# Kernel optimization log

Hardware: AMD Instinct MI355X
Metric: run time of the kernel (lower is better)

## Reference

```python
import jax, jax.numpy as jnp
import numpy as np


def _l2norm(t, axis=-1, eps=1e-12):
    # matches torch F.normalize: x / max(||x||, eps)
    n = jnp.sqrt(jnp.sum(t * t, axis=axis, keepdims=True))
    return t / jnp.maximum(n, eps)


def setup_inputs() -> dict:
    key = jax.random.key(0)
    ks = jax.random.split(key, 5)
    B, N, C, H = 16, 4096, 768, 12
    x = jax.random.normal(ks[0], (B, N, C), dtype=jnp.float32)
    Wqkv = jax.random.normal(ks[1], (C, 3 * C), dtype=jnp.float32) * (C ** -0.5)
    bqkv = jax.random.normal(ks[2], (3 * C,), dtype=jnp.float32) * 0.02
    Wproj = jax.random.normal(ks[3], (C, C), dtype=jnp.float32) * (C ** -0.5)
    bproj = jax.random.normal(ks[4], (C,), dtype=jnp.float32) * 0.02
    temperature = jnp.ones((H, 1, 1), dtype=jnp.float32)
    return {"x": x, "Wqkv": Wqkv, "bqkv": bqkv, "Wproj": Wproj,
            "bproj": bproj, "temperature": temperature}


def reference(x, Wqkv, bqkv, Wproj, bproj, temperature):
    B, N, C = x.shape
    H = temperature.shape[0]
    Dh = C // H
    qkv = x @ Wqkv + bqkv                      # [B,N,3C]
    qkv = qkv.reshape(B, N, 3, H, Dh)
    # -> [3,B,H,Dh,N] (channels-as-tokens layout)
    qkv = jnp.transpose(qkv, (2, 0, 3, 4, 1))
    q, k, v = qkv[0], qkv[1], qkv[2]           # each [B,H,Dh,N]
    q = _l2norm(q, axis=-1)
    k = _l2norm(k, axis=-1)
    # cross-covariance over channels: [B,H,Dh,Dh]
    attn = jnp.einsum('bhdn,bhen->bhde', q, k) * temperature
    attn = jax.nn.softmax(attn, axis=-1)
    out = jnp.einsum('bhde,bhen->bhdn', attn, v)  # [B,H,Dh,N]
    out = jnp.transpose(out, (0, 3, 1, 2)).reshape(B, N, C)
    return out @ Wproj + bproj
```

## Files before the change

kernel.cpp:

```cpp
#include <hip/hip_runtime.h>

typedef __bf16 bf16x8 __attribute__((ext_vector_type(8)));
typedef float  f32x4  __attribute__((ext_vector_type(4)));
typedef unsigned short u16x8 __attribute__((ext_vector_type(8)));
typedef unsigned short u16x4 __attribute__((ext_vector_type(4)));

#define MFMA16(a, b, c) __builtin_amdgcn_mfma_f32_16x16x32_bf16((a), (b), (c), 0, 0, 0)

#define GLOAD16(g, l) __builtin_amdgcn_global_load_lds( \
    (const __attribute__((address_space(1))) void*)(g),  \
    (__attribute__((address_space(3))) void*)(l), 16, 0, 0)

__device__ __forceinline__ float bf2f(unsigned short u) {
    unsigned int x = ((unsigned int)u) << 16;
    return __builtin_bit_cast(float, x);
}
__device__ __forceinline__ unsigned short f2bf(float f) {
    unsigned int x = __builtin_bit_cast(unsigned int, f);
    x = x + 0x7FFFu + ((x >> 16) & 1u);
    return (unsigned short)(x >> 16);
}
__device__ __forceinline__ bool is_f32(const unsigned short* tf) { return tf[0] == 0; }
__device__ __forceinline__ float ldscal(const void* p, int i, bool f32m) {
    return f32m ? ((const float*)p)[i] : bf2f(((const unsigned short*)p)[i]);
}

__global__ __launch_bounds__(256)
void tr_dual(const void* __restrict__ in_, unsigned short* __restrict__ xb,
             unsigned short* __restrict__ xbT, float* __restrict__ sB,
             const unsigned short* __restrict__ tf)
{
    __shared__ unsigned short T[64 * 72];
    const bool f32m = is_f32(tf);
    const int tx = blockIdx.x % 12;
    const int ty = blockIdx.x / 12;
    const int r0 = ty * 64, c0 = tx * 64;
    const int t = threadIdx.x;
#pragma unroll
    for (int s = 0; s < 2; ++s) {
        const int idx = t + s * 256;
        const int rr = idx >> 3;
        const int cc = (idx & 7) * 8;
        u16x8 v;
        if (f32m) {
            const float* inf = (const float*)in_;
            f32x4 a = *(const f32x4*)&inf[(size_t)(r0 + rr) * 768 + c0 + cc];
            f32x4 b = *(const f32x4*)&inf[(size_t)(r0 + rr) * 768 + c0 + cc + 4];
#pragma unroll
            for (int j = 0; j < 4; ++j) { v[j] = f2bf(a[j]); v[4 + j] = f2bf(b[j]); }
        } else {
            v = *(const u16x8*)&((const unsigned short*)in_)[(size_t)(r0 + rr) * 768 + c0 + cc];
        }
        *(u16x8*)&xb[(size_t)(r0 + rr) * 768 + c0 + cc] = v;
#pragma unroll
        for (int j = 0; j < 8; ++j) T[(cc + j) * 72 + rr] = v[j];
    }
    __syncthreads();
#pragma unroll
    for (int s = 0; s < 2; ++s) {
        const int idx = t + s * 256;
        const int cc = idx >> 3;
        const int rr = (idx & 7) * 8;
        u16x8 v = *(const u16x8*)&T[cc * 72 + rr];
        *(u16x8*)&xbT[(size_t)(c0 + cc) * 65536 + r0 + rr] = v;
    }
    {
        const int col = t >> 2;
        const int seg = t & 3;
        float s = 0.f;
#pragma unroll
        for (int r = 0; r < 16; ++r) s += bf2f(T[col * 72 + seg * 16 + r]);
        s += __shfl_xor(s, 1);
        s += __shfl_xor(s, 2);
        if (seg == 0) atomicAdd(&sB[(r0 >> 12) * 768 + c0 + col], s);
    }
}

__device__ __forceinline__ void tr_tile(const void* in_, unsigned short* out,
                                        int R, int C, int istride,
                                        int bid, bool f32m, unsigned short* T)
{
    const int nct = C >> 6;
    const int tx = bid % nct;
    const int ty = bid / nct;
    const int r0 = ty * 64, c0 = tx * 64;
    const int t = threadIdx.x;
#pragma unroll
    for (int s = 0; s < 2; ++s) {
        const int idx = t + s * 256;
        const int rr = idx >> 3;
        const int cc = (idx & 7) * 8;
        unsigned short v[8];
        if (f32m) {
            const float* inf = (const float*)in_;
            f32x4 a = *(const f32x4*)&inf[(size_t)(r0 + rr) * istride + c0 + cc];
            f32x4 b = *(const f32x4*)&inf[(size_t)(r0 + rr) * istride + c0 + cc + 4];
#pragma unroll
            for (int j = 0; j < 4; ++j) { v[j] = f2bf(a[j]); v[4 + j] = f2bf(b[j]); }
        } else {
            u16x8 a = *(const u16x8*)&((const unsigned short*)in_)[(size_t)(r0 + rr) * istride + c0 + cc];
#pragma unroll
            for (int j = 0; j < 8; ++j) v[j] = a[j];
        }
#pragma unroll
        for (int j = 0; j < 8; ++j) T[(cc + j) * 72 + rr] = v[j];
    }
    __syncthreads();
#pragma unroll
    for (int s = 0; s < 2; ++s) {
        const int idx = t + s * 256;
        const int cc = idx >> 3;
        const int rr = (idx & 7) * 8;
        u16x8 v = *(const u16x8*)&T[cc * 72 + rr];
        *(u16x8*)&out[(size_t)(c0 + cc) * R + r0 + rr] = v;
    }
}

__global__ __launch_bounds__(256)
void wprep(const void* __restrict__ Wqkv, const void* __restrict__ Wp,
           unsigned short* __restrict__ WqkT, unsigned short* __restrict__ Wv_bf,
           unsigned short* __restrict__ WprojT, const unsigned short* __restrict__ tf)
{
    __shared__ unsigned short T[64 * 72];
    const bool f32m = is_f32(tf);
    const int bid = blockIdx.x;
    if (bid < 288) {
        tr_tile(Wqkv, WqkT, 768, 1536, 2304, bid, f32m, T);
    } else if (bid < 576) {
        const int t = (bid - 288) * 256 + threadIdx.x;
        const int c = t / 96;
        const int e0 = (t % 96) * 8;
        u16x8 v;
        if (f32m) {
            const float* p = (const float*)Wqkv + (size_t)c * 2304 + 1536 + e0;
            f32x4 a = *(const f32x4*)p;
            f32x4 b = *(const f32x4*)(p + 4);
#pragma unroll
            for (int j = 0; j < 4; ++j) { v[j] = f2bf(a[j]); v[4 + j] = f2bf(b[j]); }
        } else {
            v = *(const u16x8*)&((const unsigned short*)Wqkv)[(size_t)c * 2304 + 1536 + e0];
        }
        *(u16x8*)&Wv_bf[(size_t)c * 768 + e0] = v;
    } else {
        tr_tile(Wp, WprojT, 768, 768, 768, bid - 576, f32m, T);
    }
}

template<int MODE>
__global__ __launch_bounds__(512, 2)
void gemm2ph(const unsigned short* __restrict__ A,
             const unsigned short* __restrict__ BT,
             const float* __restrict__ bias,
             unsigned short* __restrict__ o0,
             float* __restrict__ oF,
             const unsigned short* __restrict__ tf)
{
    constexpr int K = 768, NT = 12;
    __shared__ __align__(16) char SM[131072];
    unsigned short* lds = (unsigned short*)SM;

    const bool f32m = is_f32(tf);
    const int tid  = threadIdx.x;
    const int wave = tid >> 6;
    const int lane = tid & 63;
    const int wm   = wave >> 2;
    const int wn   = wave & 3;
    const int lr   = lane & 15;
    const int lq   = lane >> 4;

    const int per = gridDim.x >> 3;
    const int wg  = (blockIdx.x & 7) * per + (blockIdx.x >> 3);
    int b = 0, mt, nt;
    if (MODE == 4) { b = wg / 18; const int r = wg % 18; mt = r / 3; nt = r % 3; }
    else           { mt = wg / 3; nt = wg % 3; }
    const size_t m0 = (size_t)mt * 256;
    const int n0 = nt * 256;

    const unsigned short* Ab = A + m0 * K;
    const unsigned short* Bb;
    if (MODE == 1)      Bb = BT + (m0 >> 12) * (size_t)589824 + (size_t)n0 * K;
    else if (MODE == 4) Bb = BT + (size_t)b * 589824 + (size_t)n0 * K;
    else                Bb = BT + (size_t)n0 * K;

    f32x4 zero = {0.f, 0.f, 0.f, 0.f};
    f32x4 acc[8][4];
#pragma unroll
    for (int i = 0; i < 8; ++i)
#pragma unroll
        for (int j = 0; j < 4; ++j) acc[i][j] = zero;

    auto STAGE = [&](int t) {
        unsigned short* la_ = lds + (t & 1) * 32768;
        unsigned short* lb_ = la_ + 16384;
        const unsigned short* ga = Ab + t * 64;
        const unsigned short* gb = Bb + t * 64;
#pragma unroll
        for (int it = 0; it < 4; ++it) {
            const int c = it * 512 + tid;
            const int row = c >> 3;
            const int gs = (c & 7) ^ (row & 7);
            GLOAD16(ga + (size_t)row * K + gs * 8, la_ + c * 8);
        }
#pragma unroll
        for (int it = 0; it < 4; ++it) {
            const int c = it * 512 + tid;
            const int row = c >> 3;
            const int gs = (c & 7) ^ (row & 7);
            GLOAD16(gb + (size_t)row * K + gs * 8, lb_ + c * 8);
        }
    };

    STAGE(0);
    STAGE(1);

    for (int t = 0; t < NT; ++t) {
        if (t + 1 < NT) asm volatile("s_waitcnt vmcnt(8)" ::: "memory");
        else            asm volatile("s_waitcnt vmcnt(0)" ::: "memory");
        __builtin_amdgcn_s_barrier();
        __builtin_amdgcn_sched_barrier(0);

        const char* la = (const char*)(lds + (t & 1) * 32768);
        const char* lb = la + 32768;

        bf16x8 bfr[4][2];
#pragma unroll
        for (int ni = 0; ni < 4; ++ni)
#pragma unroll
            for (int ks = 0; ks < 2; ++ks) {
                const int row = wn * 64 + ni * 16 + lr;
                const int s   = ks * 4 + lq;
                bfr[ni][ks] = *(const bf16x8*)(lb + row * 128 + ((s ^ (row & 7)) << 4));
            }
#pragma unroll
        for (int mh = 0; mh < 2; ++mh) {
            bf16x8 af[4][2];
#pragma unroll
            for (int mi = 0; mi < 4; ++mi)
#pragma unroll
                for (int ks = 0; ks < 2; ++ks) {
                    const int row = wm * 128 + mh * 64 + mi * 16 + lr;
                    const int s   = ks * 4 + lq;
                    af[mi][ks] = *(const bf16x8*)(la + row * 128 + ((s ^ (row & 7)) << 4));
                }
            __builtin_amdgcn_s_setprio(1);
#pragma unroll
            for (int mi = 0; mi < 4; ++mi)
#pragma unroll
                for (int ni = 0; ni < 4; ++ni)
#pragma unroll
                    for (int ks = 0; ks < 2; ++ks)
                        acc[mh * 4 + mi][ni] = MFMA16(af[mi][ks], bfr[ni][ks], acc[mh * 4 + mi][ni]);
            __builtin_amdgcn_s_setprio(0);
        }

        __builtin_amdgcn_sched_barrier(0);
        __builtin_amdgcn_s_barrier();
        if (t + 2 < NT) STAGE(t + 2);
    }

    float bb[4];
#pragma unroll
    for (int ni = 0; ni < 4; ++ni) {
        const int col = n0 + wn * 64 + ni * 16 + lr;
        bb[ni] = (MODE == 1) ? bias[(m0 >> 12) * 768 + col] : 0.f;
    }

#pragma unroll
    for (int mi = 0; mi < 8; ++mi)
#pragma unroll
        for (int ni = 0; ni < 4; ++ni)
#pragma unroll
            for (int r = 0; r < 4; ++r) {
                const size_t row = m0 + (size_t)(wm * 128 + mi * 16 + lq * 4 + r);
                const int col = n0 + wn * 64 + ni * 16 + lr;
                const float val = acc[mi][ni][r] + bb[ni];
                if (MODE == 1) {
                    if (f32m) oF[row * 768 + col] = val;
                    else      o0[row * 768 + col] = f2bf(val);
                } else if (MODE == 2) {
                    o0[row * 768 + col] = f2bf(val);
                } else {
                    o0[(size_t)b * 1179648 + row * 768 + col] = f2bf(val);
                }
            }
}

__global__ __launch_bounds__(512, 2)
void gemm8ph(const unsigned short* __restrict__ A,
             unsigned short* __restrict__ G,
             const unsigned short* __restrict__ tf)
{
    constexpr int NT = 64;
    constexpr size_t LD = 65536;
    __shared__ __align__(16) char SM[131072];

    const int tid  = threadIdx.x;
    const int wave = tid >> 6;
    const int lane = tid & 63;
    const int wm   = wave >> 2;
    const int wn   = wave & 3;
    const int lr   = lane & 15;
    const int lq   = lane >> 4;
    const int lrh  = lr >> 1;
    const int pA   = (((lr & 1) << 2) | lq) ^ lrh;

    const int per = gridDim.x >> 3;
    const int wg  = (blockIdx.x & 7) * per + (blockIdx.x >> 3);
    const int b = wg / 9;
    const int r9 = wg % 9;
    const int mt = r9 / 3, nt = r9 % 3;
    const size_t m0 = (size_t)mt * 256;
    const int n0 = nt * 256;

    const unsigned short* Ab = A + m0 * LD + (size_t)b * 4096;
    const unsigned short* Bb = A + (size_t)n0 * LD + (size_t)b * 4096;

    f32x4 zero = {0.f, 0.f, 0.f, 0.f};
    f32x4 acc[8][4];
#pragma unroll
    for (int i = 0; i < 8; ++i)
#pragma unroll
        for (int j = 0; j < 4; ++j) acc[i][j] = zero;

    auto STAGE_EV = [&](int mat, int kh, int t) {
        const unsigned short* g = mat ? Bb : Ab;
        char* dst = SM + (t & 1) * 65536 + mat * 32768 + kh * 16384;
#pragma unroll
        for (int ev = 0; ev < 2; ++ev) {
            const int c = ev * 512 + tid;
            const int rp = c >> 3;
            const int chunk = (c & 7) ^ (rp & 7);
            const int srow = rp * 2 + (chunk >> 2);
            const int sk = kh * 32 + (chunk & 3) * 8;
            GLOAD16(g + (size_t)srow * LD + t * 64 + sk, dst + c * 16);
        }
    };

    STAGE_EV(0, 0, 0); STAGE_EV(1, 0, 0);
    STAGE_EV(0, 1, 0); STAGE_EV(1, 1, 0);
    STAGE_EV(0, 0, 1); STAGE_EV(1, 0, 1);

    bf16x8 af[4], bfr[4];

#define READ_B(ks) do { \
    _Pragma("unroll") for (int ni = 0; ni < 4; ++ni) \
        bfr[ni] = *(const bf16x8*)(lb + (ks) * 16384 + (wn * 32 + ni * 8 + lrh) * 128 + pA * 16); } while (0)
#define READ_A(mh, ks) do { \
    _Pragma("unroll") for (int mi = 0; mi < 4; ++mi) \
        af[mi] = *(const bf16x8*)(la + (ks) * 16384 + (wm * 64 + (mh) * 32 + mi * 8 + lrh) * 128 + pA * 16); } while (0)
#define MFMA_Q(mh) do { \
    _Pragma("unroll") for (int mi = 0; mi < 4; ++mi) \
    _Pragma("unroll") for (int ni = 0; ni < 4; ++ni) \
        acc[(mh) * 4 + mi][ni] = MFMA16(af[mi], bfr[ni], acc[(mh) * 4 + mi][ni]); } while (0)
#define PH_MID() do { \
    __builtin_amdgcn_sched_barrier(0); \
    __builtin_amdgcn_s_barrier(); \
    asm volatile("s_waitcnt lgkmcnt(0)" ::: "memory"); \
    __builtin_amdgcn_sched_barrier(0); } while (0)
#define PH_END() do { \
    __builtin_amdgcn_sched_barrier(0); \
    __builtin_amdgcn_s_barrier(); } while (0)

    for (int t = 0; t < NT; ++t) {
        const char* la = (const char*)SM + (t & 1) * 65536;
        const char* lb = la + 32768;

        if (t < NT - 1) asm volatile("s_waitcnt vmcnt(8)" ::: "memory");
        else            asm volatile("s_waitcnt vmcnt(4)" ::: "memory");
        __builtin_amdgcn_s_barrier();
        __builtin_amdgcn_sched_barrier(0);

        READ_B(0); READ_A(0, 0);
        if (t + 1 < NT) STAGE_EV(0, 1, t + 1);
        PH_MID();
        __builtin_amdgcn_s_setprio(1); MFMA_Q(0); __builtin_amdgcn_s_setprio(0);
        PH_END();

        READ_A(1, 0);
        if (t + 1 < NT) STAGE_EV(1, 1, t + 1);
        if (t < NT - 1) asm volatile("s_waitcnt vmcnt(8)" ::: "memory");
        else            asm volatile("s_waitcnt vmcnt(0)" ::: "memory");
        PH_MID();
        __builtin_amdgcn_s_setprio(1); MFMA_Q(1); __builtin_amdgcn_s_setprio(0);
        PH_END();

        READ_B(1); READ_A(0, 1);
        if (t + 2 < NT) STAGE_EV(0, 0, t + 2);
        PH_MID();
        __builtin_amdgcn_s_setprio(1); MFMA_Q(0); __builtin_amdgcn_s_setprio(0);
        PH_END();

        READ_A(1, 1);
        if (t + 2 < NT) STAGE_EV(1, 0, t + 2);
        PH_MID();
        __builtin_amdgcn_s_setprio(1); MFMA_Q(1); __builtin_amdgcn_s_setprio(0);
        PH_END();
    }
#undef READ_B
#undef READ_A
#undef MFMA_Q
#undef PH_MID
#undef PH_END

#pragma unroll
    for (int mi = 0; mi < 8; ++mi)
#pragma unroll
        for (int ni = 0; ni < 4; ++ni)
#pragma unroll
            for (int r = 0; r < 4; ++r) {
                const size_t row = m0 + (size_t)(wm * 128 + mi * 16 + lq * 4 + r);
                const int col = n0 + wn * 64 + ni * 16 + lr;
                G[(size_t)b * 589824 + row * 768 + col] = f2bf(acc[mi][ni][r]);
            }
}

__global__ __launch_bounds__(256)
void attn2(const unsigned short* __restrict__ P,
           const unsigned short* __restrict__ WqkT,
           const float* __restrict__ s,
           const void* __restrict__ bqkv,
           const unsigned short* __restrict__ tf,
           unsigned short* __restrict__ attnT)
{
    __shared__ float S[64][64];
    __shared__ float nq[64], nk[64], uq[64], uk[64];
    __shared__ float sb[768];
    __shared__ float bkv[64];
    const bool f32m = is_f32(tf);
    const int bh = blockIdx.x;
    const int b = bh / 12, h = bh % 12;
    const unsigned short* Pq = P + (size_t)b * 1179648 + (size_t)(h * 64) * 768;
    const unsigned short* Pk = Pq + 768 * 768;
    const unsigned short* Wq = WqkT + (size_t)(h * 64) * 768;
    const unsigned short* Wk = Wq + 768 * 768;
    const int tid = threadIdx.x;
    const int wave = tid >> 6;
    const int lane = tid & 63;
    const int lr = lane & 15;
    const int lq = lane >> 4;

    for (int i = tid; i < 768; i += 256) sb[i] = s[b * 768 + i];
    if (tid < 64) bkv[tid] = ldscal(bqkv, 768 + h * 64 + tid, f32m);

    f32x4 zero = {0.f, 0.f, 0.f, 0.f};
    f32x4 acc[4][4];
#pragma unroll
    for (int i = 0; i < 4; ++i)
#pragma unroll
        for (int j = 0; j < 4; ++j) acc[i][j] = zero;

    for (int ks = 0; ks < 6; ++ks) {
        const int j0 = wave * 192 + ks * 32 + lq * 8;
        u16x8 qa[4], ka[4];
#pragma unroll
        for (int mi = 0; mi < 4; ++mi)
            qa[mi] = *(const u16x8*)&Pq[(size_t)(mi * 16 + lr) * 768 + j0];
#pragma unroll
        for (int ni = 0; ni < 4; ++ni)
            ka[ni] = *(const u16x8*)&Wk[(size_t)(ni * 16 + lr) * 768 + j0];
#pragma unroll
        for (int mi = 0; mi < 4; ++mi)
#pragma unroll
            for (int ni = 0; ni < 4; ++ni)
                acc[mi][ni] = MFMA16(__builtin_bit_cast(bf16x8, qa[mi]),
                                     __builtin_bit_cast(bf16x8, ka[ni]),
                                     acc[mi][ni]);
    }
    __syncthreads();

    for (int ww = 0; ww < 4; ++ww) {
        if (wave == ww) {
#pragma unroll
            for (int mi = 0; mi < 4; ++mi)
#pragma unroll
                for (int ni = 0; ni < 4; ++ni)
#pragma unroll
                    for (int r = 0; r < 4; ++r) {
                        const int d = mi * 16 + lq * 4 + r;
                        const int e = ni * 16 + lr;
                        if (ww == 0) S[d][e] = acc[mi][ni][r];
                        else         S[d][e] += acc[mi][ni][r];
                    }
        }
        __syncthreads();
    }

    const int d  = tid >> 2;
    const int q4 = tid & 3;
    {
        const unsigned short* pqr = Pq + (size_t)d * 768 + q4 * 192;
        const unsigned short* wqr = Wq + (size_t)d * 768 + q4 * 192;
        const unsigned short* pkr = Pk + (size_t)d * 768 + q4 * 192;
        const unsigned short* wkr = Wk + (size_t)d * 768 + q4 * 192;
        float a_nq = 0.f, a_uq = 0.f, a_nk = 0.f, a_uk = 0.f;
        for (int i = 0; i < 24; ++i) {
            u16x8 vp = *(const u16x8*)&pqr[i * 8];
            u16x8 vw = *(const u16x8*)&wqr[i * 8];
            u16x8 kp = *(const u16x8*)&pkr[i * 8];
            u16x8 kw = *(const u16x8*)&wkr[i * 8];
#pragma unroll
            for (int j = 0; j < 8; ++j) {
                const float wqv = bf2f(vw[j]);
                const float wkv = bf2f(kw[j]);
                const float sj = sb[q4 * 192 + i * 8 + j];
                a_nq += bf2f(vp[j]) * wqv;
                a_uq += sj * wqv;
                a_nk += bf2f(kp[j]) * wkv;
                a_uk += sj * wkv;
            }
        }
        a_nq += __shfl_xor(a_nq, 1); a_nq += __shfl_xor(a_nq, 2);
        a_uq += __shfl_xor(a_uq, 1); a_uq += __shfl_xor(a_uq, 2);
        a_nk += __shfl_xor(a_nk, 1); a_nk += __shfl_xor(a_nk, 2);
        a_uk += __shfl_xor(a_uk, 1); a_uk += __shfl_xor(a_uk, 2);
        if (q4 == 0) { nq[d] = a_nq; uq[d] = a_uq; nk[d] = a_nk; uk[d] = a_uk; }
    }
    __syncthreads();

    const float tv  = f32m ? ((const float*)tf)[h] : bf2f(tf[h]);
    const float bqd = ldscal(bqkv, h * 64 + d, f32m);
    const float uqd = uq[d];
    const float nqf = nq[d] + 2.f * bqd * uqd + 4096.f * bqd * bqd;
    const float qn  = fmaxf(sqrtf(fmaxf(nqf, 0.f)), 1e-12f);
    float vals[16];
    float mx = -1e30f;
#pragma unroll
    for (int i = 0; i < 16; ++i) {
        const int e = q4 * 16 + i;
        const float bke = bkv[e];
        const float nkf = nk[e] + 2.f * bke * uk[e] + 4096.f * bke * bke;
        const float kn  = fmaxf(sqrtf(fmaxf(nkf, 0.f)), 1e-12f);
        const float sv  = S[d][e] + bqd * uk[e] + uqd * bke + 4096.f * bqd * bke;
        const float val = sv / (qn * kn) * tv;
        vals[i] = val;
        mx = fmaxf(mx, val);
    }
    mx = fmaxf(mx, __shfl_xor(mx, 1));
    mx = fmaxf(mx, __shfl_xor(mx, 2));
    float sum = 0.f;
#pragma unroll
    for (int i = 0; i < 16; ++i) { vals[i] = __expf(vals[i] - mx); sum += vals[i]; }
    sum += __shfl_xor(sum, 1);
    sum += __shfl_xor(sum, 2);
    const float inv = 1.0f / sum;
#pragma unroll
    for (int i = 0; i < 16; ++i) {
        const int e = q4 * 16 + i;
        attnT[(size_t)bh * 4096 + e * 64 + d] = f2bf(vals[i] * inv);
    }
}

__global__ __launch_bounds__(512)
void mb_build(const unsigned short* __restrict__ attnT,
              const unsigned short* __restrict__ WprojT,
              unsigned short* __restrict__ MbT)
{
    const int bh = blockIdx.x;
    const int b = bh / 12, h = bh % 12;
    const int tid = threadIdx.x;
    const int wave = tid >> 6;
    const int lane = tid & 63;
    const unsigned short* At = attnT + (size_t)bh * 4096;

    f32x4 zero = {0.f, 0.f, 0.f, 0.f};
    f32x4 acc[4][6];
#pragma unroll
    for (int i = 0; i < 4; ++i)
#pragma unroll
        for (int j = 0; j < 6; ++j) acc[i][j] = zero;

    const int lr  = lane & 15;
    const int lk8 = (lane >> 4) * 8;

#pragma unroll
    for (int ks = 0; ks < 2; ++ks) {
        bf16x8 af[4], bfr[6];
#pragma unroll
        for (int mi = 0; mi < 4; ++mi)
            af[mi] = *(const bf16x8*)&At[(mi * 16 + lr) * 64 + ks * 32 + lk8];
#pragma unroll
        for (int ni = 0; ni < 6; ++ni) {
            const int j = wave * 96 + ni * 16 + lr;
            bfr[ni] = *(const bf16x8*)&WprojT[(size_t)j * 768 + h * 64 + ks * 32 + lk8];
        }
#pragma unroll
        for (int mi = 0; mi < 4; ++mi)
#pragma unroll
            for (int ni = 0; ni < 6; ++ni)
                acc[mi][ni] = MFMA16(af[mi], bfr[ni], acc[mi][ni]);
    }

#pragma unroll
    for (int mi = 0; mi < 4; ++mi)
#pragma unroll
        for (int ni = 0; ni < 6; ++ni) {
            const int e = mi * 16 + (lane >> 4) * 4;
            const int j = wave * 96 + ni * 16 + lr;
            u16x4 pk;
#pragma unroll
            for (int r = 0; r < 4; ++r) pk[r] = f2bf(acc[mi][ni][r]);
            *(u16x4*)&MbT[(size_t)b * 589824 + (size_t)j * 768 + h * 64 + e] = pk;
        }
}

__global__ __launch_bounds__(256)
void beff_k(const unsigned short* __restrict__ MbT,
            const void* __restrict__ bqkv, const void* __restrict__ bp,
            float* __restrict__ beff, const unsigned short* __restrict__ tf)
{
    __shared__ float bv[768];
    const bool f32m = is_f32(tf);
    for (int i = threadIdx.x; i < 768; i += 256) bv[i] = ldscal(bqkv, 1536 + i, f32m);
    __syncthreads();
    const int t = blockIdx.x * 256 + threadIdx.x;
    const int b = t / 768, j = t % 768;
    float s = ldscal(bp, j, f32m);
    const unsigned short* row = MbT + (size_t)b * 589824 + (size_t)j * 768;
    for (int e8 = 0; e8 < 96; ++e8) {
        u16x8 m = *(const u16x8*)&row[e8 * 8];
#pragma unroll
        for (int jj = 0; jj < 8; ++jj) s += bf2f(m[jj]) * bv[e8 * 8 + jj];
    }
    beff[t] = s;
}

extern "C" void kernel_launch(void* const* d_in, const int* in_sizes, int n_in,
                              void* d_out, int out_size, void* d_ws, size_t ws_size,
                              hipStream_t stream)
{
    const void* x    = d_in[0];
    const void* Wqkv = d_in[1];
    const void* bqkv = d_in[2];
    const void* Wp   = d_in[3];
    const void* bp   = d_in[4];
    const unsigned short* tf = (const unsigned short*)d_in[5];

    char* w = (char*)d_ws;
    unsigned short* xbT    = (unsigned short*)(w);
    unsigned short* xb     = (unsigned short*)(w + 100663296);
    unsigned short* G      = (unsigned short*)(w + 201326592);
    unsigned short* P      = (unsigned short*)(w + 220200960);
    unsigned short* PT     = (unsigned short*)(w + 257949696);
    unsigned short* MbT    = (unsigned short*)(w + 276824064);
    unsigned short* WqkT   = (unsigned short*)(w + 295698432);
    unsigned short* Wv_bf  = (unsigned short*)(w + 298057728);
    unsigned short* WprojT = (unsigned short*)(w + 299237376);
    unsigned short* attnT  = (unsigned short*)(w + 300417024);
    float*          sB     = (float*)(w + 301989888);
    float*          beff   = (float*)(w + 302039040);

    hipMemsetAsync(sB, 0, 16 * 768 * sizeof(float), stream);
    tr_dual<<<dim3(12288), dim3(256), 0, stream>>>(x, xb, xbT, sB, tf);
    wprep<<<dim3(720), dim3(256), 0, stream>>>(Wqkv, Wp, WqkT, Wv_bf, WprojT, tf);

    gemm8ph<<<dim3(144), dim3(512), 0, stream>>>(xbT, G, tf);
    gemm2ph<4><<<dim3(288), dim3(512), 0, stream>>>(WqkT, G, nullptr, P, nullptr, tf);
    attn2<<<dim3(192), dim3(256), 0, stream>>>(P, WqkT, sB, bqkv, tf, attnT);
    mb_build<<<dim3(192), dim3(512), 0, stream>>>(attnT, WprojT, MbT);
    gemm2ph<2><<<dim3(144), dim3(512), 0, stream>>>(MbT, Wv_bf, nullptr, PT, nullptr, tf);
    beff_k<<<dim3(48), dim3(256), 0, stream>>>(MbT, bqkv, bp, beff, tf);
    gemm2ph<1><<<dim3(768), dim3(512), 0, stream>>>(xb, PT, beff,
        (unsigned short*)d_out, (float*)d_out, tf);
}
```

Before: 450.2 us.

## Shrink GEMM tiles and LDS footprint to raise occupancy and grid size

Swaps the 256x256 Gram GEMM (gemm8ph, 144 blocks) for a simpler 128x128 tile kernel with 256 threads and 64KB LDS, launched as 576 blocks. The generic GEMM moves to 128x256 tiles with a K-step of 32, 48KB LDS and launch bounds of 4 blocks per CU, which doubles the grid for every mode. The goal is to fill all CUs on mi355x and hide latency through occupancy rather than large register tiles. In exchange, each tile reuses less data and does more barrier and load-issue work per FLOP, and the 4-phase staged pipeline of the old Gram kernel is dropped.

```diff
diff --git a/kernel.cpp b/kernel.cpp
--- a/kernel.cpp
+++ b/kernel.cpp
@@ -146,18 +146,126 @@
     }
 }
 
+__global__ __launch_bounds__(256, 2)
+void gemmG(const unsigned short* __restrict__ A, unsigned short* __restrict__ G)
+{
+    constexpr int NT = 64;
+    constexpr size_t LD = 65536;
+    __shared__ __align__(16) char SM[65536];
+    unsigned short* lds = (unsigned short*)SM;
+
+    const int tid  = threadIdx.x;
+    const int wave = tid >> 6;
+    const int lane = tid & 63;
+    const int wm   = wave >> 1;
+    const int wn   = wave & 1;
+    const int lr   = lane & 15;
+    const int lq   = lane >> 4;
+
+    const int per = gridDim.x >> 3;
+    const int wg  = (blockIdx.x & 7) * per + (blockIdx.x >> 3);
+    const int b = wg / 36;
+    const int r36 = wg % 36;
+    const int mt = r36 / 6, nt = r36 % 6;
+    const size_t m0 = (size_t)mt * 128;
+    const int n0 = nt * 128;
+
+    const unsigned short* Ab = A + m0 * LD + (size_t)b * 4096;
+    const unsigned short* Bb = A + (size_t)n0 * LD + (size_t)b * 4096;
+
+    f32x4 zero = {0.f, 0.f, 0.f, 0.f};
+    f32x4 acc[4][4];
+#pragma unroll
+    for (int i = 0; i < 4; ++i)
+#pragma unroll
+        for (int j = 0; j < 4; ++j) acc[i][j] = zero;
+
+    auto STAGE = [&](int t) {
+        unsigned short* la_ = lds + (t & 1) * 16384;
+        unsigned short* lb_ = la_ + 8192;
+#pragma unroll
+        for (int it = 0; it < 4; ++it) {
+            const int c = it * 256 + tid;
+            const int row = c >> 3;
+            const int gs = (c & 7) ^ (row & 7);
+            GLOAD16(Ab + (size_t)row * LD + t * 64 + gs * 8, la_ + c * 8);
+        }
+#pragma unroll
+        for (int it = 0; it < 4; ++it) {
+            const int c = it * 256 + tid;
+            const int row = c >> 3;
+            const int gs = (c & 7) ^ (row & 7);
+            GLOAD16(Bb + (size_t)row * LD + t * 64 + gs * 8, lb_ + c * 8);
+        }
+    };
+
+    STAGE(0);
+    STAGE(1);
+
+    for (int t = 0; t < NT; ++t) {
+        if (t + 1 < NT) asm volatile("s_waitcnt vmcnt(8)" ::: "memory");
+        else            asm volatile("s_waitcnt vmcnt(0)" ::: "memory");
+        __builtin_amdgcn_s_barrier();
+        __builtin_amdgcn_sched_barrier(0);
+
+        const char* la = (const char*)(lds + (t & 1) * 16384);
+        const char* lb = la + 16384;
+
+        bf16x8 bfr[4][2], af[4][2];
+#pragma unroll
+        for (int ni = 0; ni < 4; ++ni)
+#pragma unroll
+            for (int ks = 0; ks < 2; ++ks) {
+                const int row = wn * 64 + ni * 16 + lr;
+                const int s   = ks * 4 + lq;
+                bfr[ni][ks] = *(const bf16x8*)(lb + row * 128 + ((s ^ (row & 7)) << 4));
+            }
+#pragma unroll
+        for (int mi = 0; mi < 4; ++mi)
+#pragma unroll
+            for (int ks = 0; ks < 2; ++ks) {
+                const int row = wm * 64 + mi * 16 + lr;
+                const int s   = ks * 4 + lq;
+                af[mi][ks] = *(const bf16x8*)(la + row * 128 + ((s ^ (row & 7)) << 4));
+            }
+        __builtin_amdgcn_s_setprio(1);
+#pragma unroll
+        for (int mi = 0; mi < 4; ++mi)
+#pragma unroll
+            for (int ni = 0; ni < 4; ++ni)
+#pragma unroll
+                for (int ks = 0; ks < 2; ++ks)
+                    acc[mi][ni] = MFMA16(af[mi][ks], bfr[ni][ks], acc[mi][ni]);
+        __builtin_amdgcn_s_setprio(0);
+
+        __builtin_amdgcn_sched_barrier(0);
+        __builtin_amdgcn_s_barrier();
+        if (t + 2 < NT) STAGE(t + 2);
+    }
+
+#pragma unroll
+    for (int mi = 0; mi < 4; ++mi)
+#pragma unroll
+        for (int ni = 0; ni < 4; ++ni)
+#pragma unroll
+            for (int r = 0; r < 4; ++r) {
+                const size_t row = m0 + (size_t)(wm * 64 + mi * 16 + lq * 4 + r);
+                const int col = n0 + wn * 64 + ni * 16 + lr;
+                G[(size_t)b * 589824 + row * 768 + col] = f2bf(acc[mi][ni][r]);
+            }
+}
+
 template<int MODE>
-__global__ __launch_bounds__(512, 2)
-void gemm2ph(const unsigned short* __restrict__ A,
-             const unsigned short* __restrict__ BT,
-             const float* __restrict__ bias,
-             unsigned short* __restrict__ o0,
-             float* __restrict__ oF,
-             const unsigned short* __restrict__ tf)
-{
-    constexpr int K = 768, NT = 12;
-    __shared__ __align__(16) char SM[131072];
-    unsigned short* lds = (unsigned short*)SM;
+__global__ __launch_bounds__(512, 4)
+void gemmH(const unsigned short* __restrict__ A,
+           const unsigned short* __restrict__ BT,
+           const float* __restrict__ bias,
+           unsigned short* __restrict__ o0,
+           float* __restrict__ oF,
+           const unsigned short* __restrict__ tf)
+{
+    constexpr int K = 768, NT = 24;
+    __shared__ __align__(16) char SM[49152];
 
     const bool f32m = is_f32(tf);
     const int tid  = threadIdx.x;
@@ -171,9 +279,9 @@
     const int per = gridDim.x >> 3;
     const int wg  = (blockIdx.x & 7) * per + (blockIdx.x >> 3);
     int b = 0, mt, nt;
-    if (MODE == 4) { b = wg / 18; const int r = wg % 18; mt = r / 3; nt = r % 3; }
+    if (MODE == 4) { b = wg / 36; const int r = wg % 36; mt = r / 3; nt = r % 3; }
     else           { mt = wg / 3; nt = wg % 3; }
-    const size_t m0 = (size_t)mt * 256;
+    const size_t m0 = (size_t)mt * 128;
     const int n0 = nt * 256;
 
     const unsigned short* Ab = A + m0 * K;
@@ -183,30 +291,30 @@
     else                Bb = BT + (size_t)n0 * K;
 
     f32x4 zero = {0.f, 0.f, 0.f, 0.f};
-    f32x4 acc[8][4];
-#pragma unroll
-    for (int i = 0; i < 8; ++i)
+    f32x4 acc[4][4];
+#pragma unroll
+    for (int i = 0; i < 4; ++i)
 #pragma unroll
         for (int j = 0; j < 4; ++j) acc[i][j] = zero;
 
     auto STAGE = [&](int t) {
-        unsigned short* la_ = lds + (t & 1) * 32768;
-        unsigned short* lb_ = la_ + 16384;
-        const unsigned short* ga = Ab + t * 64;
-        const unsigned short* gb = Bb + t * 64;
-#pragma unroll
-        for (int it = 0; it < 4; ++it) {
-            const int c = it * 512 + tid;
-            const int row = c >> 3;
-            const int gs = (c & 7) ^ (row & 7);
-            GLOAD16(ga + (size_t)row * K + gs * 8, la_ + c * 8);
-        }
-#pragma unroll
-        for (int it = 0; it < 4; ++it) {
-            const int c = it * 512 + tid;
-            const int row = c >> 3;
-            const int gs = (c & 7) ^ (row & 7);
-            GLOAD16(gb + (size_t)row * K + gs * 8, lb_ + c * 8);
+        char* base = SM + (t & 1) * 24576;
+        {
+            const int c = tid;
+            const int rp = c >> 3;
+            const int ch = (c & 7) ^ (rp & 7);
+            const int srow = rp * 2 + (ch >> 2);
+            const int sk = (ch & 3) * 8;
+            GLOAD16(Ab + (size_t)srow * K + t * 32 + sk, base + c * 16);
+        }
+#pragma unroll
+        for (int ev = 0; ev < 2; ++ev) {
+            const int c = ev * 512 + tid;
+            const int rp = c >> 3;
+            const int ch = (c & 7) ^ (rp & 7);
+            const int srow = rp * 2 + (ch >> 2);
+            const int sk = (ch & 3) * 8;
+            GLOAD16(Bb + (size_t)srow * K + t * 32 + sk, base + 8192 + c * 16);
         }
     };
 
@@ -214,44 +322,36 @@
     STAGE(1);
 
     for (int t = 0; t < NT; ++t) {
-        if (t + 1 < NT) asm volatile("s_waitcnt vmcnt(8)" ::: "memory");
+        if (t + 1 < NT) asm volatile("s_waitcnt vmcnt(3)" ::: "memory");
         else            asm volatile("s_waitcnt vmcnt(0)" ::: "memory");
         __builtin_amdgcn_s_barrier();
         __builtin_amdgcn_sched_barrier(0);
 
-        const char* la = (const char*)(lds + (t & 1) * 32768);
-        const char* lb = la + 32768;
-
-        bf16x8 bfr[4][2];
-#pragma unroll
-        for (int ni = 0; ni < 4; ++ni)
-#pragma unroll
-            for (int ks = 0; ks < 2; ++ks) {
-                const int row = wn * 64 + ni * 16 + lr;
-                const int s   = ks * 4 + lq;
-                bfr[ni][ks] = *(const bf16x8*)(lb + row * 128 + ((s ^ (row & 7)) << 4));
-            }
-#pragma unroll
-        for (int mh = 0; mh < 2; ++mh) {
-            bf16x8 af[4][2];
-#pragma unroll
-            for (int mi = 0; mi < 4; ++mi)
-#pragma unroll
-                for (int ks = 0; ks < 2; ++ks) {
-                    const int row = wm * 128 + mh * 64 + mi * 16 + lr;
-                    const int s   = ks * 4 + lq;
-                    af[mi][ks] = *(const bf16x8*)(la + row * 128 + ((s ^ (row & 7)) << 4));
-                }
-            __builtin_amdgcn_s_setprio(1);
-#pragma unroll
-            for (int mi = 0; mi < 4; ++mi)
-#pragma unroll
-                for (int ni = 0; ni < 4; ++ni)
-#pragma unroll
-                    for (int ks = 0; ks < 2; ++ks)
-                        acc[mh * 4 + mi][ni] = MFMA16(af[mi][ks], bfr[ni][ks], acc[mh * 4 + mi][ni]);
-            __builtin_amdgcn_s_setprio(0);
-        }
+        const char* la = SM + (t & 1) * 24576;
+        const char* lb = la + 8192;
+
+        bf16x8 af[4], bfr[4];
+#pragma unroll
+        for (int ni = 0; ni < 4; ++ni) {
+            const int row = wn * 64 + ni * 16 + lr;
+            const int rp = row >> 1;
+            const int ch = (row & 1) * 4 + lq;
+            bfr[ni] = *(const bf16x8*)(lb + rp * 128 + ((ch ^ (rp & 7)) << 4));
+        }
+#pragma unroll
+        for (int mi = 0; mi < 4; ++mi) {
+            const int row = wm * 64 + mi * 16 + lr;
+            const int rp = row >> 1;
+            const int ch = (row & 1) * 4 + lq;
+            af[mi] = *(const bf16x8*)(la + rp * 128 + ((ch ^ (rp & 7)) << 4));
+        }
+        __builtin_amdgcn_s_setprio(1);
+#pragma unroll
+        for (int mi = 0; mi < 4; ++mi)
+#pragma unroll
+            for (int ni = 0; ni < 4; ++ni)
+                acc[mi][ni] = MFMA16(af[mi], bfr[ni], acc[mi][ni]);
+        __builtin_amdgcn_s_setprio(0);
 
         __builtin_amdgcn_sched_barrier(0);
         __builtin_amdgcn_s_barrier();
@@ -266,12 +366,12 @@
     }
 
 #pragma unroll
-    for (int mi = 0; mi < 8; ++mi)
+    for (int mi = 0; mi < 4; ++mi)
 #pragma unroll
         for (int ni = 0; ni < 4; ++ni)
 #pragma unroll
             for (int r = 0; r < 4; ++r) {
-                const size_t row = m0 + (size_t)(wm * 128 + mi * 16 + lq * 4 + r);
+                const size_t row = m0 + (size_t)(wm * 64 + mi * 16 + lq * 4 + r);
                 const int col = n0 + wn * 64 + ni * 16 + lr;
                 const float val = acc[mi][ni][r] + bb[ni];
                 if (MODE == 1) {
@@ -282,135 +382,6 @@
                 } else {
                     o0[(size_t)b * 1179648 + row * 768 + col] = f2bf(val);
                 }
-            }
-}
-
-__global__ __launch_bounds__(512, 2)
-void gemm8ph(const unsigned short* __restrict__ A,
-             unsigned short* __restrict__ G,
-             const unsigned short* __restrict__ tf)
-{
-    constexpr int NT = 64;
-    constexpr size_t LD = 65536;
-    __shared__ __align__(16) char SM[131072];
-
-    const int tid  = threadIdx.x;
-    const int wave = tid >> 6;
-    const int lane = tid & 63;
-    const int wm   = wave >> 2;
-    const int wn   = wave & 3;
-    const int lr   = lane & 15;
-    const int lq   = lane >> 4;
-    const int lrh  = lr >> 1;
-    const int pA   = (((lr & 1) << 2) | lq) ^ lrh;
-
-    const int per = gridDim.x >> 3;
-    const int wg  = (blockIdx.x & 7) * per + (blockIdx.x >> 3);
-    const int b = wg / 9;
-    const int r9 = wg % 9;
-    const int mt = r9 / 3, nt = r9 % 3;
-    const size_t m0 = (size_t)mt * 256;
-    const int n0 = nt * 256;
-
-    const unsigned short* Ab = A + m0 * LD + (size_t)b * 4096;
-    const unsigned short* Bb = A + (size_t)n0 * LD + (size_t)b * 4096;
-
-    f32x4 zero = {0.f, 0.f, 0.f, 0.f};
-    f32x4 acc[8][4];
-#pragma unroll
-    for (int i = 0; i < 8; ++i)
-#pragma unroll
-        for (int j = 0; j < 4; ++j) acc[i][j] = zero;
-
-    auto STAGE_EV = [&](int mat, int kh, int t) {
-        const unsigned short* g = mat ? Bb : Ab;
-        char* dst = SM + (t & 1) * 65536 + mat * 32768 + kh * 16384;
-#pragma unroll
-        for (int ev = 0; ev < 2; ++ev) {
-            const int c = ev * 512 + tid;
-            const int rp = c >> 3;
-            const int chunk = (c & 7) ^ (rp & 7);
-            const int srow = rp * 2 + (chunk >> 2);
-            const int sk = kh * 32 + (chunk & 3) * 8;
-            GLOAD16(g + (size_t)srow * LD + t * 64 + sk, dst + c * 16);
-        }
-    };
-
-    STAGE_EV(0, 0, 0); STAGE_EV(1, 0, 0);
-    STAGE_EV(0, 1, 0); STAGE_EV(1, 1, 0);
-    STAGE_EV(0, 0, 1); STAGE_EV(1, 0, 1);
-
-    bf16x8 af[4], bfr[4];
-
-#define READ_B(ks) do { \
-    _Pragma("unroll") for (int ni = 0; ni < 4; ++ni) \
-        bfr[ni] = *(const bf16x8*)(lb + (ks) * 16384 + (wn * 32 + ni * 8 + lrh) * 128 + pA * 16); } while (0)
-#define READ_A(mh, ks) do { \
-    _Pragma("unroll") for (int mi = 0; mi < 4; ++mi) \
-        af[mi] = *(const bf16x8*)(la + (ks) * 16384 + (wm * 64 + (mh) * 32 + mi * 8 + lrh) * 128 + pA * 16); } while (0)
-#define MFMA_Q(mh) do { \
-    _Pragma("unroll") for (int mi = 0; mi < 4; ++mi) \
-    _Pragma("unroll") for (int ni = 0; ni < 4; ++ni) \
-        acc[(mh) * 4 + mi][ni] = MFMA16(af[mi], bfr[ni], acc[(mh) * 4 + mi][ni]); } while (0)
-#define PH_MID() do { \
-    __builtin_amdgcn_sched_barrier(0); \
-    __builtin_amdgcn_s_barrier(); \
-    asm volatile("s_waitcnt lgkmcnt(0)" ::: "memory"); \
-    __builtin_amdgcn_sched_barrier(0); } while (0)
-#define PH_END() do { \
-    __builtin_amdgcn_sched_barrier(0); \
-    __builtin_amdgcn_s_barrier(); } while (0)
-
-    for (int t = 0; t < NT; ++t) {
-        const char* la = (const char*)SM + (t & 1) * 65536;
-        const char* lb = la + 32768;
-
-        if (t < NT - 1) asm volatile("s_waitcnt vmcnt(8)" ::: "memory");
-        else            asm volatile("s_waitcnt vmcnt(4)" ::: "memory");
-        __builtin_amdgcn_s_barrier();
-        __builtin_amdgcn_sched_barrier(0);
-
-        READ_B(0); READ_A(0, 0);
-        if (t + 1 < NT) STAGE_EV(0, 1, t + 1);
-        PH_MID();
-        __builtin_amdgcn_s_setprio(1); MFMA_Q(0); __builtin_amdgcn_s_setprio(0);
-        PH_END();
-
-        READ_A(1, 0);
-        if (t + 1 < NT) STAGE_EV(1, 1, t + 1);
-        if (t < NT - 1) asm volatile("s_waitcnt vmcnt(8)" ::: "memory");
-        else            asm volatile("s_waitcnt vmcnt(0)" ::: "memory");
-        PH_MID();
-        __builtin_amdgcn_s_setprio(1); MFMA_Q(1); __builtin_amdgcn_s_setprio(0);
-        PH_END();
-
-        READ_B(1); READ_A(0, 1);
-        if (t + 2 < NT) STAGE_EV(0, 0, t + 2);
-        PH_MID();
-        __builtin_amdgcn_s_setprio(1); MFMA_Q(0); __builtin_amdgcn_s_setprio(0);
-        PH_END();
-
-        READ_A(1, 1);
-        if (t + 2 < NT) STAGE_EV(1, 0, t + 2);
-        PH_MID();
-        __builtin_amdgcn_s_setprio(1); MFMA_Q(1); __builtin_amdgcn_s_setprio(0);
-        PH_END();
-    }
-#undef READ_B
-#undef READ_A
-#undef MFMA_Q
-#undef PH_MID
-#undef PH_END
-
-#pragma unroll
-    for (int mi = 0; mi < 8; ++mi)
-#pragma unroll
-        for (int ni = 0; ni < 4; ++ni)
-#pragma unroll
-            for (int r = 0; r < 4; ++r) {
-                const size_t row = m0 + (size_t)(wm * 128 + mi * 16 + lq * 4 + r);
-                const int col = n0 + wn * 64 + ni * 16 + lr;
-                G[(size_t)b * 589824 + row * 768 + col] = f2bf(acc[mi][ni][r]);
             }
 }
 
@@ -653,12 +624,12 @@
     tr_dual<<<dim3(12288), dim3(256), 0, stream>>>(x, xb, xbT, sB, tf);
     wprep<<<dim3(720), dim3(256), 0, stream>>>(Wqkv, Wp, WqkT, Wv_bf, WprojT, tf);
 
-    gemm8ph<<<dim3(144), dim3(512), 0, stream>>>(xbT, G, tf);
-    gemm2ph<4><<<dim3(288), dim3(512), 0, stream>>>(WqkT, G, nullptr, P, nullptr, tf);
+    gemmG<<<dim3(576), dim3(256), 0, stream>>>(xbT, G);
+    gemmH<4><<<dim3(576), dim3(512), 0, stream>>>(WqkT, G, nullptr, P, nullptr, tf);
     attn2<<<dim3(192), dim3(256), 0, stream>>>(P, WqkT, sB, bqkv, tf, attnT);
     mb_build<<<dim3(192), dim3(512), 0, stream>>>(attnT, WprojT, MbT);
-    gemm2ph<2><<<dim3(144), dim3(512), 0, stream>>>(MbT, Wv_bf, nullptr, PT, nullptr, tf);
+    gemmH<2><<<dim3(288), dim3(512), 0, stream>>>(MbT, Wv_bf, nullptr, PT, nullptr, tf);
     beff_k<<<dim3(48), dim3(256), 0, stream>>>(MbT, bqkv, bp, beff, tf);
-    gemm2ph<1><<<dim3(768), dim3(512), 0, stream>>>(xb, PT, beff,
+    gemmH<1><<<dim3(1536), dim3(512), 0, stream>>>(xb, PT, beff,
         (unsigned short*)d_out, (float*)d_out, tf);
 }
```

Result: no change. 445.0 us (-1.1%).
